# Kernel tuning notes

Measured on AMD Instinct MI355X. Metric: run time of the kernel, lower is better.

The kernel has to match this reference:

```python
import jax, jax.numpy as jnp
import numpy as np

LAMBDA_FGW = 0.5
TAU_KL = 0.1
N_OUTER = 5
N_SINKHORN = 10
DIM = 512


def _pdist(a, b):
    # sqrt(clamp(||a-b||^2, 1e-6)) computed via expansion (avoids BxKxMxD temp)
    n2 = ((a * a).sum(-1)[:, :, None] + (b * b).sum(-1)[:, None, :]
          - 2.0 * jnp.einsum('bkd,bmd->bkm', a, b))
    return jnp.sqrt(jnp.clip(n2, 1e-6, None))


def setup_inputs() -> dict:
    key = jax.random.key(0)
    ks = jax.random.split(key, 10)
    B, K, M, D = 256, 128, 128, DIM
    inp = {
        'sq': jax.random.normal(ks[0], (B, K, D), jnp.float32),
        'sr': jax.random.normal(ks[1], (B, M, D), jnp.float32),
        'mask_q': jax.random.uniform(ks[2], (B, K), jnp.float32),
        'mask_r': jax.random.uniform(ks[3], (B, M), jnp.float32),
        'centroids_q': jax.random.normal(ks[4], (B, K, D), jnp.float32),
        'centroids_r': jax.random.normal(ks[5], (B, M, D), jnp.float32),
        'W1': jax.random.normal(ks[6], (D, D), jnp.float32) * 0.02,
        'b1': jnp.zeros((D,), jnp.float32),
        'W2': jax.random.normal(ks[7], (D, D), jnp.float32) * 0.02,
        'b2': jnp.zeros((D,), jnp.float32),
        'log_eps': jnp.asarray(np.log(0.05), jnp.float32),
    }
    return inp


def reference(sq, sr, mask_q, mask_r, centroids_q, centroids_r, W1, b1, W2, b2, log_eps):
    proj = lambda x: jax.nn.relu(x @ W1 + b1) @ W2 + b2
    pq, pr = proj(sq), proj(sr)
    C = _pdist(pq, pr)                      # [B,K,M]
    Sq = _pdist(centroids_q, centroids_q)   # [B,K,K]
    Sr = _pdist(centroids_r, centroids_r)   # [B,M,M]

    mu = mask_q / (mask_q.sum(-1, keepdims=True) + 1e-8)  # [B,K]
    nu = mask_r / (mask_r.sum(-1, keepdims=True) + 1e-8)  # [B,M]
    T = mu[:, :, None] * nu[:, None, :]

    eps = jnp.clip(jnp.exp(log_eps), 0.01, 0.5)
    rho = TAU_KL / (TAU_KL + eps)
    log_mu = jnp.log(jnp.clip(mu, 1e-8, None))
    log_nu = jnp.log(jnp.clip(nu, 1e-8, None))
    Sq2, Sr2 = Sq * Sq, Sr * Sr

    C_fgw = C
    for _ in range(N_OUTER):
        t1 = jnp.einsum('bkl,bl->bk', Sq2, T.sum(2))[:, :, None]
        t2 = jnp.einsum('bm,bmn->bn', T.sum(1), Sr2)[:, None, :]
        L_gw = t1 + t2 - 2.0 * jnp.einsum('bkl,blm->bkm', Sq, jnp.einsum('blm,bmn->bln', T, Sr))
        C_fgw = (1.0 - LAMBDA_FGW) * C + LAMBDA_FGW * L_gw
        log_K = -C_fgw / eps
        log_u = jnp.zeros_like(mu)
        log_v = jnp.zeros_like(nu)
        for _ in range(N_SINKHORN):
            log_u = rho * (log_mu - jax.nn.logsumexp(log_K + log_v[:, None, :], axis=2))
            log_v = rho * (log_nu - jax.nn.logsumexp(log_K + log_u[:, :, None], axis=1))
        T = jnp.exp(log_u[:, :, None] + log_K + log_v[:, None, :])

    cost = (T * C_fgw).sum((-1, -2))
    similarity = jax.nn.sigmoid(-cost)
    return similarity, T, C, cost
```

## Files before the change

### kernel.cpp

```cpp
#include <hip/hip_runtime.h>
#include <math.h>

typedef unsigned short u16;
typedef __attribute__((ext_vector_type(4))) float f32x4;
typedef __attribute__((ext_vector_type(8))) short bf16x8;
typedef __attribute__((ext_vector_type(4))) unsigned short u16x4;
typedef __attribute__((ext_vector_type(8))) unsigned short u16x8;

#define DEVI static __device__ __forceinline__

DEVI float b2f(u16 u){ union{float f; unsigned i;} v; v.i = ((unsigned)u)<<16; return v.f; }
DEVI u16 f2b(float f){ union{float f; unsigned i;} v; v.f=f;
  unsigned r = v.i + 0x7fffu + ((v.i>>16)&1u); return (u16)(r>>16); }

DEVI void gload_lds16(const void* g, void* l){
  __builtin_amdgcn_global_load_lds((const __attribute__((address_space(1))) void*)g,
                                   (__attribute__((address_space(3))) void*)l, 16, 0, 0);
}

DEVI f32x4 vmax4(f32x4 a, f32x4 b){
  f32x4 r; r[0]=fmaxf(a[0],b[0]); r[1]=fmaxf(a[1],b[1]);
  r[2]=fmaxf(a[2],b[2]); r[3]=fmaxf(a[3],b[3]); return r;
}

__global__ void prepw_k(const float* __restrict__ W, u16* __restrict__ Wt){
  int id = blockIdx.x*256 + threadIdx.x;
  int k = id>>9, c = id&511;
  Wt[c*512 + k] = f2b(W[id]);
}

__global__ void cvt_k(const float* __restrict__ src, u16* __restrict__ dst,
                      float* __restrict__ norms, int nrows){
  int gw = (int)((blockIdx.x*blockDim.x + threadIdx.x)>>6);
  int lane = threadIdx.x & 63;
  if (gw >= nrows) return;
  const float* s = src + (size_t)gw*512;
  u16* d = dst + (size_t)gw*512;
  float acc = 0.f;
  #pragma unroll
  for (int q=0;q<2;q++){
    f32x4 v = *(const f32x4*)(s + q*256 + lane*4);
    u16x4 u;
    #pragma unroll
    for (int e=0;e<4;e++){
      u16 b = f2b(v[e]); u[e] = b;
      float fv = b2f(b); acc += fv*fv;
    }
    *(u16x4*)(d + q*256 + lane*4) = u;
  }
  #pragma unroll
  for (int off=1;off<64;off<<=1) acc += __shfl_xor(acc, off);
  if (norms != nullptr && lane==0) norms[gw] = acc;
}

__global__ void normb_k(const u16* __restrict__ src, float* __restrict__ norms, int nrows){
  int gw = (int)((blockIdx.x*blockDim.x + threadIdx.x)>>6);
  int lane = threadIdx.x & 63;
  if (gw >= nrows) return;
  const u16* s = src + (size_t)gw*512;
  u16x8 v = *(const u16x8*)(s + lane*8);
  float acc = 0.f;
  #pragma unroll
  for (int e=0;e<8;e++){ float f = b2f(v[e]); acc += f*f; }
  #pragma unroll
  for (int off=1;off<64;off<<=1) acc += __shfl_xor(acc, off);
  if (lane==0) norms[gw] = acc;
}

template<int ACT>
__global__ __launch_bounds__(256) void gemm_k(const u16* __restrict__ X,
    const u16* __restrict__ Wt, const float* __restrict__ bias, u16* __restrict__ OUT){
  __shared__ __align__(16) u16 sA[128*64];
  __shared__ __align__(16) u16 sB[128*64];
  const int tid = threadIdx.x, wave = tid>>6, lane = tid&63;
  const int bid = (blockIdx.x&7)*256 + (blockIdx.x>>3);
  const int rblk = bid>>2, cb = (bid&3)<<7;
  const u16* Xb = X + (size_t)rblk*(128*512);
  const u16* Wb = Wt + (size_t)cb*512;
  const int lrow = lane&15, lg = lane>>4, wr = wave>>1, wc = wave&1;
  f32x4 acc[4][4] = {};
  for (int s=0;s<8;s++){
    const int k0 = s<<6;
    #pragma unroll
    for (int q=0;q<4;q++){
      const int i = (wave<<2)+q;
      const int row = (i<<3) + (lane>>3);
      const int cd = (lane&7) ^ (row&7);
      gload_lds16(Xb + row*512 + k0 + (cd<<3), sA + i*512);
      gload_lds16(Wb + row*512 + k0 + (cd<<3), sB + i*512);
    }
    __syncthreads();
    #pragma unroll
    for (int kh=0;kh<2;kh++){
      bf16x8 a_[4], b_[4];
      #pragma unroll
      for (int i=0;i<4;i++){
        const int ra = (wr<<6)+(i<<4)+lrow;
        a_[i] = *(const bf16x8*)(sA + ra*64 + ((((kh<<2)+lg)^(ra&7))<<3));
        const int rb = (wc<<6)+(i<<4)+lrow;
        b_[i] = *(const bf16x8*)(sB + rb*64 + ((((kh<<2)+lg)^(rb&7))<<3));
      }
      #pragma unroll
      for (int i=0;i<4;i++)
        #pragma unroll
        for (int j=0;j<4;j++)
          acc[i][j] = __builtin_amdgcn_mfma_f32_16x16x32_bf16(a_[i], b_[j], acc[i][j], 0,0,0);
    }
    __syncthreads();
  }
  #pragma unroll
  for (int j=0;j<4;j++){
    const int col = cb + (wc<<6) + (j<<4) + lrow;
    const float bv = bias[col];
    #pragma unroll
    for (int i=0;i<4;i++){
      const int row0 = (rblk<<7) + (wr<<6) + (i<<4) + (lg<<2);
      #pragma unroll
      for (int r=0;r<4;r++){
        float v = acc[i][j][r] + bv;
        if (ACT) v = fmaxf(v, 0.f);
        OUT[(size_t)(row0+r)*512 + col] = f2b(v);
      }
    }
  }
}

template<int MODE>
__global__ __launch_bounds__(256) void pdist_k(const u16* __restrict__ Xa,
    const u16* __restrict__ Xb2, const float* __restrict__ na, const float* __restrict__ nb,
    float* __restrict__ OUT, float* __restrict__ S2t, char* __restrict__ SHL){
  __shared__ __align__(16) u16 sA[128*64];
  __shared__ __align__(16) u16 sB[128*64];
  const int tid = threadIdx.x, wave = tid>>6, lane = tid&63;
  const int b = blockIdx.x;
  const u16* Ab = Xa + (size_t)b*(128*512);
  const u16* Bb = Xb2 + (size_t)b*(128*512);
  const int lrow = lane&15, lg = lane>>4, wr = wave>>1, wc = wave&1;
  f32x4 acc[4][4] = {};
  for (int s=0;s<8;s++){
    const int k0 = s<<6;
    #pragma unroll
    for (int q=0;q<4;q++){
      const int i = (wave<<2)+q;
      const int row = (i<<3) + (lane>>3);
      const int cd = (lane&7) ^ (row&7);
      gload_lds16(Ab + row*512 + k0 + (cd<<3), sA + i*512);
      gload_lds16(Bb + row*512 + k0 + (cd<<3), sB + i*512);
    }
    __syncthreads();
    #pragma unroll
    for (int kh=0;kh<2;kh++){
      bf16x8 a_[4], b_[4];
      #pragma unroll
      for (int i=0;i<4;i++){
        const int ra = (wr<<6)+(i<<4)+lrow;
        a_[i] = *(const bf16x8*)(sA + ra*64 + ((((kh<<2)+lg)^(ra&7))<<3));
        const int rb = (wc<<6)+(i<<4)+lrow;
        b_[i] = *(const bf16x8*)(sB + rb*64 + ((((kh<<2)+lg)^(rb&7))<<3));
      }
      #pragma unroll
      for (int i=0;i<4;i++)
        #pragma unroll
        for (int j=0;j<4;j++)
          acc[i][j] = __builtin_amdgcn_mfma_f32_16x16x32_bf16(a_[i], b_[j], acc[i][j], 0,0,0);
    }
    __syncthreads();
  }
  #pragma unroll
  for (int j=0;j<4;j++){
    const int col = (wc<<6)+(j<<4)+lrow;
    const float nbv = nb[b*128+col];
    #pragma unroll
    for (int i=0;i<4;i++){
      const int row0 = (wr<<6)+(i<<4)+(lg<<2);
      float sv[4];
      #pragma unroll
      for (int r=0;r<4;r++){
        float n2 = na[b*128+row0+r] + nbv - 2.0f*acc[i][j][r];
        sv[r] = sqrtf(fmaxf(n2, 1e-6f));
      }
      if (MODE==0){
        #pragma unroll
        for (int r=0;r<4;r++)
          OUT[(size_t)b*16384 + (size_t)(row0+r)*128 + col] = sv[r];
      } else {
        u16x4 hi4, lo4; f32x4 s2q;
        #pragma unroll
        for (int r=0;r<4;r++){
          u16 h = f2b(sv[r]); hi4[r] = h;
          lo4[r] = f2b(sv[r] - b2f(h));
          s2q[r] = sv[r]*sv[r];
        }
        const int sa = col*256 + ((((row0>>3)^col)&15)<<4) + ((row0&7)<<1);
        char* base = SHL + (size_t)b*65536;
        *(u16x4*)(base + sa) = hi4;
        *(u16x4*)(base + 32768 + sa) = lo4;
        *(f32x4*)(S2t + (size_t)b*16384 + col*128 + row0) = s2q;
      }
    }
  }
}

__global__ void prep_k(const float* __restrict__ mask_q, const float* __restrict__ mask_r,
                       float* __restrict__ lmu, float* __restrict__ lnu,
                       float* __restrict__ mu, float* __restrict__ nu){
  int b = blockIdx.x, t = threadIdx.x;
  __shared__ float red[4];
  float mq = mask_q[b*128+t], mr = mask_r[b*128+t];
  float s1 = mq, s2 = mr;
  #pragma unroll
  for (int off=1;off<64;off<<=1){ s1 += __shfl_xor(s1,off); s2 += __shfl_xor(s2,off); }
  if ((t&63)==0){ red[t>>6] = s1; red[2+(t>>6)] = s2; }
  __syncthreads();
  float sumq = red[0]+red[1], sumr = red[2]+red[3];
  float muv = mq/(sumq+1e-8f), nuv = mr/(sumr+1e-8f);
  lmu[b*128+t] = __logf(fmaxf(muv,1e-8f));
  lnu[b*128+t] = __logf(fmaxf(nuv,1e-8f));
  mu[b*128+t] = muv;
  nu[b*128+t] = nuv;
}

__global__ __launch_bounds__(512,1) void fgw_loop_k(
    const char* __restrict__ SQHL, const char* __restrict__ SRHL,
    const float* __restrict__ SQ2, const float* __restrict__ SR2,
    const float* __restrict__ C_g,
    const float* __restrict__ MU, const float* __restrict__ NU,
    const float* __restrict__ LMU, const float* __restrict__ LNU,
    const float* __restrict__ log_eps,
    float* __restrict__ T_out, float* __restrict__ cost_out, float* __restrict__ sim_out)
{
  __shared__ __align__(16) char bufT[65536];
  __shared__ __align__(16) char bufS[65536];
  __shared__ __align__(16) float avs[128], bvs[128], t1s[128], t2s[128];
  __shared__ __align__(16) float lus[128], lvs[128];
  __shared__ float redc[8];

  const int b = blockIdx.x, tid = threadIdx.x;
  const int w = tid>>6, lane = tid&63, l15 = lane&15, lg = lane>>4;
  const char* SqHLb = SQHL + (size_t)b*65536;
  const char* SrHLb = SRHL + (size_t)b*65536;
  const float* Sq2b = SQ2 + (size_t)b*16384;
  const float* Sr2b = SR2 + (size_t)b*16384;
  const float* Cb   = C_g + (size_t)b*16384;
  const float* MUb  = MU + b*128;
  const float* NUb  = NU + b*128;

  float eps = __expf(log_eps[0]); eps = fminf(fmaxf(eps,0.01f),0.5f);
  const float rho = 0.1f/(0.1f+eps), inve = 1.0f/eps;

  const int kR = 16*w + l15;
  const int nC = kR;
  const int n0 = 16*w + 4*lg;
  const float lmuR = LMU[b*128+kR];
  const float lnuC = LNU[b*128+nC];
  const float muR  = MUb[kR];
  const float nuC  = NUb[nC];

  const int rowA256 = (16*w + l15)*256;
  const int glo2 = lg ^ (l15 & 3);
  const int ghi2 = l15 & 12;
  const int wtail = l15*256 + ((((2*w + (lg>>1)) ^ l15)&15)<<4) + ((lg&1)<<3);

  f32x4 lkR[8], lkC[8];
  float luR = 0.f, lvC = 0.f;

  for (int outer=0; outer<5; outer++){
    #pragma unroll
    for (int r2=0;r2<8;r2++)
      gload_lds16(SrHLb + r2*8192 + tid*16, bufS + r2*8192 + tid*16);
    {
      f32x4 avp = {0.f,0.f,0.f,0.f};
      float bvp = 0.f;
      #pragma unroll
      for (int q=0;q<8;q++){
        f32x4 TRq, TCq;
        if (outer==0){
          const f32x4 nu4 = *(const f32x4*)(NUb + 16*q + 4*lg);
          const f32x4 mu4 = *(const f32x4*)(MUb + 16*q + 4*lg);
          TRq = muR*nu4;
          TCq = mu4*nuC;
        } else {
          const f32x4 lv4 = *(const f32x4*)&lvs[16*q+4*lg];
          const f32x4 lu4 = *(const f32x4*)&lus[16*q+4*lg];
          #pragma unroll
          for (int e=0;e<4;e++){
            TRq[e] = __expf(lkR[q][e] + luR + lv4[e]);
            TCq[e] = __expf(lkC[q][e] + lu4[e] + lvC);
          }
        }
        u16x4 hi4, lo4;
        #pragma unroll
        for (int e=0;e<4;e++){
          u16 h = f2b(TRq[e]); hi4[e] = h;
          lo4[e] = f2b(TRq[e] - b2f(h));
        }
        const int sa = kR*256 + ((((2*q+(lg>>1)) ^ l15)&15)<<4) + ((lg&1)<<3);
        *(u16x4*)(bufT + sa) = hi4;
        *(u16x4*)(bufT + 32768 + sa) = lo4;
        avp += TRq;
        bvp += TCq[0]+TCq[1]+TCq[2]+TCq[3];
      }
      float av = avp[0]+avp[1]+avp[2]+avp[3];
      av += __shfl_xor(av,16); av += __shfl_xor(av,32);
      bvp += __shfl_xor(bvp,16); bvp += __shfl_xor(bvp,32);
      if (lg==0){ avs[kR] = av; bvs[nC] = bvp; }
    }
    __syncthreads();

    {
      const int k = tid>>2, q = tid&3;
      const float* r1 = Sq2b + k*128 + q*32;
      const float* r2p = Sr2b + k*128 + q*32;
      f32x4 a1 = {0.f,0.f,0.f,0.f}, a2 = {0.f,0.f,0.f,0.f};
      #pragma unroll
      for (int i=0;i<8;i++){
        a1 += (*(const f32x4*)(r1+4*i)) * (*(const f32x4*)(avs+q*32+4*i));
        a2 += (*(const f32x4*)(r2p+4*i)) * (*(const f32x4*)(bvs+q*32+4*i));
      }
      float s1 = a1[0]+a1[1]+a1[2]+a1[3];
      float s2 = a2[0]+a2[1]+a2[2]+a2[3];
      s1 += __shfl_xor(s1,1); s1 += __shfl_xor(s1,2);
      s2 += __shfl_xor(s2,1); s2 += __shfl_xor(s2,2);
      if (q==0){ t1s[k]=s1; t2s[k]=s2; }
    }
    f32x4 acc1[8] = {};
    #pragma unroll
    for (int qt=0;qt<4;qt++){
      const int colOff = (((4*qt) ^ ghi2) | glo2) << 4;
      const bf16x8 ahi = *(const bf16x8*)(bufT + rowA256 + colOff);
      const bf16x8 alo = *(const bf16x8*)(bufT + 32768 + rowA256 + colOff);
      const int bbase = l15*256 + colOff;
      #pragma unroll
      for (int nt=0;nt<8;nt++){
        const bf16x8 bhi = *(const bf16x8*)(bufS + nt*4096 + bbase);
        const bf16x8 blo = *(const bf16x8*)(bufS + 32768 + nt*4096 + bbase);
        acc1[nt] = __builtin_amdgcn_mfma_f32_16x16x32_bf16(ahi, bhi, acc1[nt], 0,0,0);
        acc1[nt] = __builtin_amdgcn_mfma_f32_16x16x32_bf16(ahi, blo, acc1[nt], 0,0,0);
        acc1[nt] = __builtin_amdgcn_mfma_f32_16x16x32_bf16(alo, bhi, acc1[nt], 0,0,0);
      }
    }
    __syncthreads();
    #pragma unroll
    for (int r2=0;r2<8;r2++)
      gload_lds16(SqHLb + r2*8192 + tid*16, bufS + r2*8192 + tid*16);
    #pragma unroll
    for (int nt=0;nt<8;nt++){
      u16x4 hi4, lo4;
      #pragma unroll
      for (int r=0;r<4;r++){
        u16 h = f2b(acc1[nt][r]); hi4[r] = h;
        lo4[r] = f2b(acc1[nt][r] - b2f(h));
      }
      const int sa = nt*4096 + wtail;
      *(u16x4*)(bufT + sa) = hi4;
      *(u16x4*)(bufT + 32768 + sa) = lo4;
    }
    __syncthreads();
    f32x4 acc2[8] = {};
    #pragma unroll
    for (int qt=0;qt<4;qt++){
      const int colOff = (((4*qt) ^ ghi2) | glo2) << 4;
      const bf16x8 ahi = *(const bf16x8*)(bufT + rowA256 + colOff);
      const bf16x8 alo = *(const bf16x8*)(bufT + 32768 + rowA256 + colOff);
      const int bbase = l15*256 + colOff;
      #pragma unroll
      for (int kt=0;kt<8;kt++){
        const bf16x8 bhi = *(const bf16x8*)(bufS + kt*4096 + bbase);
        const bf16x8 blo = *(const bf16x8*)(bufS + 32768 + kt*4096 + bbase);
        acc2[kt] = __builtin_amdgcn_mfma_f32_16x16x32_bf16(ahi, bhi, acc2[kt], 0,0,0);
        acc2[kt] = __builtin_amdgcn_mfma_f32_16x16x32_bf16(ahi, blo, acc2[kt], 0,0,0);
        acc2[kt] = __builtin_amdgcn_mfma_f32_16x16x32_bf16(alo, bhi, acc2[kt], 0,0,0);
      }
    }
    f32x4 lkf[8];
    {
      const f32x4 t24 = *(const f32x4*)&t2s[n0];
      #pragma unroll
      for (int kt=0;kt<8;kt++){
        const int k = 16*kt + l15;
        const f32x4 c4 = *(const f32x4*)(Cb + k*128 + n0);
        lkf[kt] = -inve*(0.5f*c4 + 0.5f*(t1s[k] + t24 - 2.0f*acc2[kt]));
      }
    }
    __syncthreads();
    #pragma unroll
    for (int kt=0;kt<8;kt++){
      const int row = 16*kt + l15;
      const int gp = ((4*w+lg) ^ (row&31)) & 31;
      *(f32x4*)(bufT + row*512 + gp*16) = lkf[kt];
      #pragma unroll
      for (int e=0;e<4;e++){
        const int n = n0 + e;
        const int gt = ((4*kt + (l15>>2)) ^ (n&31)) & 31;
        *(float*)(bufS + n*512 + gt*16 + (l15&3)*4) = lkf[kt][e];
      }
    }
    __syncthreads();
    #pragma unroll
    for (int q=0;q<8;q++){
      const int g1 = ((4*q+lg) ^ (kR&31)) & 31;
      lkR[q] = *(const f32x4*)(bufT + kR*512 + g1*16);
      const int g2 = ((4*q+lg) ^ (nC&31)) & 31;
      lkC[q] = *(const f32x4*)(bufS + nC*512 + g2*16);
    }
    for (int it=0; it<10; it++){
      f32x4 y[8];
      #pragma unroll
      for (int q=0;q<8;q++){
        if (it==0) y[q] = lkR[q];
        else       y[q] = lkR[q] + *(const f32x4*)&lvs[16*q+4*lg];
      }
      f32x4 m4 = y[0];
      #pragma unroll
      for (int q=1;q<8;q++) m4 = vmax4(m4, y[q]);
      float mx = fmaxf(fmaxf(m4[0],m4[1]), fmaxf(m4[2],m4[3]));
      mx = fmaxf(mx, __shfl_xor(mx,16));
      mx = fmaxf(mx, __shfl_xor(mx,32));
      f32x4 s4 = {0.f,0.f,0.f,0.f};
      #pragma unroll
      for (int q=0;q<8;q++){
        #pragma unroll
        for (int e=0;e<4;e++) s4[e] += __expf(y[q][e]-mx);
      }
      float s = s4[0]+s4[1]+s4[2]+s4[3];
      s += __shfl_xor(s,16); s += __shfl_xor(s,32);
      luR = rho*(lmuR - (mx + __logf(s)));
      if (lg==0) lus[kR] = luR;
      __syncthreads();
      #pragma unroll
      for (int q=0;q<8;q++)
        y[q] = lkC[q] + *(const f32x4*)&lus[16*q+4*lg];
      m4 = y[0];
      #pragma unroll
      for (int q=1;q<8;q++) m4 = vmax4(m4, y[q]);
      mx = fmaxf(fmaxf(m4[0],m4[1]), fmaxf(m4[2],m4[3]));
      mx = fmaxf(mx, __shfl_xor(mx,16));
      mx = fmaxf(mx, __shfl_xor(mx,32));
      s4 = (f32x4){0.f,0.f,0.f,0.f};
      #pragma unroll
      for (int q=0;q<8;q++){
        #pragma unroll
        for (int e=0;e<4;e++) s4[e] += __expf(y[q][e]-mx);
      }
      s = s4[0]+s4[1]+s4[2]+s4[3];
      s += __shfl_xor(s,16); s += __shfl_xor(s,32);
      lvC = rho*(lnuC - (mx + __logf(s)));
      if (lg==0) lvs[nC] = lvC;
      __syncthreads();
    }
    if (outer==4){
      float cp = 0.f;
      float* Tb = T_out + (size_t)b*16384;
      #pragma unroll
      for (int q=0;q<8;q++){
        const f32x4 lv4 = *(const f32x4*)&lvs[16*q+4*lg];
        f32x4 t;
        #pragma unroll
        for (int e=0;e<4;e++) t[e] = __expf(lkR[q][e] + luR + lv4[e]);
        *(f32x4*)(Tb + kR*128 + 16*q + 4*lg) = t;
        const f32x4 p = t*lkR[q];
        cp += p[0]+p[1]+p[2]+p[3];
      }
      cp *= -eps;
      #pragma unroll
      for (int off=1;off<64;off<<=1) cp += __shfl_xor(cp, off);
      if (lane==0) redc[w] = cp;
      __syncthreads();
      if (tid==0){
        float tot = 0.f;
        #pragma unroll
        for (int w2=0;w2<8;w2++) tot += redc[w2];
        cost_out[b] = tot;
        sim_out[b]  = 1.0f/(1.0f + __expf(tot));
      }
    }
  }
}

extern "C" void kernel_launch(void* const* d_in, const int* in_sizes, int n_in,
                              void* d_out, int out_size, void* d_ws, size_t ws_size,
                              hipStream_t stream){
  const float* sq      = (const float*)d_in[0];
  const float* sr      = (const float*)d_in[1];
  const float* mask_q  = (const float*)d_in[2];
  const float* mask_r  = (const float*)d_in[3];
  const float* cq      = (const float*)d_in[4];
  const float* cr      = (const float*)d_in[5];
  const float* W1      = (const float*)d_in[6];
  const float* b1      = (const float*)d_in[7];
  const float* W2      = (const float*)d_in[8];
  const float* b2      = (const float*)d_in[9];
  const float* log_eps = (const float*)d_in[10];

  float* out  = (float*)d_out;
  float* sim  = out;
  float* Tm   = out + 256;
  float* Cm   = Tm + 4194304;
  float* cost = Cm + 4194304;

  char* ws = (char*)d_ws;
  size_t off = 0;
  auto alloc = [&](size_t bytes)->void*{ void* p = ws + off; off += (bytes+255)&~(size_t)255; return p; };
  u16*   SQB = (u16*)  alloc(33554432);
  u16*   SRB = (u16*)  alloc(33554432);
  u16*   HQ  = (u16*)  alloc(33554432);
  u16*   HR  = (u16*)  alloc(33554432);
  u16*   W1T = (u16*)  alloc(524288);
  u16*   W2T = (u16*)  alloc(524288);
  float* NP  = (float*)alloc(262144);
  float* NCQ = (float*)alloc(131072);
  float* NCR = (float*)alloc(131072);
  float* LMU = (float*)alloc(131072);
  float* LNU = (float*)alloc(131072);
  float* MUA = (float*)alloc(131072);
  float* NUA = (float*)alloc(131072);
  (void)ws_size; (void)in_sizes; (void)n_in; (void)out_size;

  u16* PQ  = SQB;
  u16* CQB = HQ;
  u16* CRB = HR;

  float* SQ2  = (float*)((char*)SQB);
  float* SR2  = (float*)((char*)SQB + 16777216);
  char*  SQHL = (char*)SQB + 33554432;
  char*  SRHL = (char*)SQB + 50331648;

  prepw_k<<<1024,256,0,stream>>>(W1, W1T);
  prepw_k<<<1024,256,0,stream>>>(W2, W2T);
  cvt_k<<<8192,256,0,stream>>>(sq, SQB, nullptr, 32768);
  cvt_k<<<8192,256,0,stream>>>(sr, SRB, nullptr, 32768);
  gemm_k<1><<<2048,256,0,stream>>>(SQB, W1T, b1, HQ);
  gemm_k<0><<<2048,256,0,stream>>>(HQ, W2T, b2, PQ);
  normb_k<<<16384,256,0,stream>>>(PQ, NP, 65536);
  cvt_k<<<8192,256,0,stream>>>(cq, CQB, NCQ, 32768);
  cvt_k<<<8192,256,0,stream>>>(cr, CRB, NCR, 32768);
  pdist_k<0><<<256,256,0,stream>>>(PQ, PQ + (size_t)32768*512, NP, NP + 32768,
                                   Cm, nullptr, nullptr);
  pdist_k<1><<<256,256,0,stream>>>(CQB, CQB, NCQ, NCQ, nullptr, SQ2, SQHL);
  pdist_k<1><<<256,256,0,stream>>>(CRB, CRB, NCR, NCR, nullptr, SR2, SRHL);
  prep_k<<<256,128,0,stream>>>(mask_q, mask_r, LMU, LNU, MUA, NUA);
  fgw_loop_k<<<256,512,0,stream>>>(SQHL, SRHL, SQ2, SR2, Cm, MUA, NUA, LMU, LNU,
                                   log_eps, Tm, cost, sim);
}
```

Before: 477.4 us.

## Fuse MLP projection into one kernel and widen FGW loop to 1024 threads

```diff
diff --git a/kernel.cpp b/kernel.cpp
--- a/kernel.cpp
+++ b/kernel.cpp
@@ -26,7 +26,7 @@
 __global__ void prepw_k(const float* __restrict__ W, u16* __restrict__ Wt){
   int id = blockIdx.x*256 + threadIdx.x;
   int k = id>>9, c = id&511;
-  Wt[c*512 + k] = f2b(W[id]);
+  Wt[c*512 + (((k>>3)^(c&15))<<3) + (k&7)] = f2b(W[id]);
 }
 
 __global__ void cvt_k(const float* __restrict__ src, u16* __restrict__ dst,
@@ -50,78 +50,115 @@
   }
   #pragma unroll
   for (int off=1;off<64;off<<=1) acc += __shfl_xor(acc, off);
-  if (norms != nullptr && lane==0) norms[gw] = acc;
-}
-
-__global__ void normb_k(const u16* __restrict__ src, float* __restrict__ norms, int nrows){
-  int gw = (int)((blockIdx.x*blockDim.x + threadIdx.x)>>6);
-  int lane = threadIdx.x & 63;
-  if (gw >= nrows) return;
-  const u16* s = src + (size_t)gw*512;
-  u16x8 v = *(const u16x8*)(s + lane*8);
-  float acc = 0.f;
-  #pragma unroll
-  for (int e=0;e<8;e++){ float f = b2f(v[e]); acc += f*f; }
-  #pragma unroll
-  for (int off=1;off<64;off<<=1) acc += __shfl_xor(acc, off);
   if (lane==0) norms[gw] = acc;
 }
 
-template<int ACT>
-__global__ __launch_bounds__(256) void gemm_k(const u16* __restrict__ X,
-    const u16* __restrict__ Wt, const float* __restrict__ bias, u16* __restrict__ OUT){
-  __shared__ __align__(16) u16 sA[128*64];
-  __shared__ __align__(16) u16 sB[128*64];
-  const int tid = threadIdx.x, wave = tid>>6, lane = tid&63;
-  const int bid = (blockIdx.x&7)*256 + (blockIdx.x>>3);
-  const int rblk = bid>>2, cb = (bid&3)<<7;
-  const u16* Xb = X + (size_t)rblk*(128*512);
-  const u16* Wb = Wt + (size_t)cb*512;
-  const int lrow = lane&15, lg = lane>>4, wr = wave>>1, wc = wave&1;
-  f32x4 acc[4][4] = {};
-  for (int s=0;s<8;s++){
-    const int k0 = s<<6;
-    #pragma unroll
-    for (int q=0;q<4;q++){
-      const int i = (wave<<2)+q;
-      const int row = (i<<3) + (lane>>3);
-      const int cd = (lane&7) ^ (row&7);
-      gload_lds16(Xb + row*512 + k0 + (cd<<3), sA + i*512);
-      gload_lds16(Wb + row*512 + k0 + (cd<<3), sB + i*512);
-    }
-    __syncthreads();
-    #pragma unroll
-    for (int kh=0;kh<2;kh++){
-      bf16x8 a_[4], b_[4];
-      #pragma unroll
-      for (int i=0;i<4;i++){
-        const int ra = (wr<<6)+(i<<4)+lrow;
-        a_[i] = *(const bf16x8*)(sA + ra*64 + ((((kh<<2)+lg)^(ra&7))<<3));
-        const int rb = (wc<<6)+(i<<4)+lrow;
-        b_[i] = *(const bf16x8*)(sB + rb*64 + ((((kh<<2)+lg)^(rb&7))<<3));
-      }
+__global__ __launch_bounds__(512) void mlp_k(
+    const float* __restrict__ sq, const float* __restrict__ sr,
+    const u16* __restrict__ W1S, const u16* __restrict__ W2S,
+    const float* __restrict__ b1, const float* __restrict__ b2,
+    u16* __restrict__ P, float* __restrict__ NP)
+{
+  __shared__ __align__(16) u16 sW[2][16384];
+  __shared__ __align__(16) u16 sH[64*512];
+  __shared__ float sB1[512], sB2[512];
+  __shared__ float npart[8][16];
+
+  const int tid = threadIdx.x, w = tid>>6, lane = tid&63;
+  const int l15 = lane&15, lg = lane>>4;
+  const int rt = w>>1, par = w&1;
+  const int row0 = blockIdx.x*64;
+  const float* Xb = (blockIdx.x < 512) ? sq + (size_t)row0*512
+                                       : sr + (size_t)(row0-32768)*512;
+  if (tid<512){ sB1[tid] = b1[tid]; sB2[tid] = b2[tid]; }
+
+  bf16x8 Xfr[16];
+  {
+    const float* xr = Xb + (size_t)(16*rt + l15)*512;
+    #pragma unroll
+    for (int kc=0;kc<16;kc++){
+      f32x4 a = *(const f32x4*)(xr + 32*kc + 8*lg);
+      f32x4 c2 = *(const f32x4*)(xr + 32*kc + 8*lg + 4);
+      u16x8 t;
+      t[0]=f2b(a[0]); t[1]=f2b(a[1]); t[2]=f2b(a[2]); t[3]=f2b(a[3]);
+      t[4]=f2b(c2[0]); t[5]=f2b(c2[1]); t[6]=f2b(c2[2]); t[7]=f2b(c2[3]);
+      Xfr[kc] = *(bf16x8*)&t;
+    }
+  }
+
+  #pragma unroll
+  for (int i=0;i<4;i++)
+    gload_lds16((const char*)W1S + i*8192 + tid*16, (char*)sW[0] + i*8192 + tid*16);
+  __syncthreads();
+  for (int p=0;p<16;p++){
+    if (p<15){
       #pragma unroll
       for (int i=0;i<4;i++)
-        #pragma unroll
-        for (int j=0;j<4;j++)
-          acc[i][j] = __builtin_amdgcn_mfma_f32_16x16x32_bf16(a_[i], b_[j], acc[i][j], 0,0,0);
-    }
-    __syncthreads();
-  }
-  #pragma unroll
-  for (int j=0;j<4;j++){
-    const int col = cb + (wc<<6) + (j<<4) + lrow;
-    const float bv = bias[col];
-    #pragma unroll
-    for (int i=0;i<4;i++){
-      const int row0 = (rblk<<7) + (wr<<6) + (i<<4) + (lg<<2);
-      #pragma unroll
-      for (int r=0;r<4;r++){
-        float v = acc[i][j][r] + bv;
-        if (ACT) v = fmaxf(v, 0.f);
-        OUT[(size_t)(row0+r)*512 + col] = f2b(v);
-      }
-    }
+        gload_lds16((const char*)W1S + (p+1)*32768 + i*8192 + tid*16,
+                    (char*)sW[(p+1)&1] + i*8192 + tid*16);
+    }
+    f32x4 acc = {0.f,0.f,0.f,0.f};
+    const u16* bw = sW[p&1] + (16*par + l15)*512;
+    #pragma unroll
+    for (int kc=0;kc<16;kc++){
+      bf16x8 bf = *(const bf16x8*)(bw + (((4*kc+lg)^l15)<<3));
+      acc = __builtin_amdgcn_mfma_f32_16x16x32_bf16(Xfr[kc], bf, acc, 0,0,0);
+    }
+    const int c = 32*p + 16*par + l15;
+    const float bv = sB1[c];
+    #pragma unroll
+    for (int r=0;r<4;r++){
+      float h = fmaxf(acc[r]+bv, 0.f);
+      const int m = 16*rt + 4*lg + r;
+      sH[m*512 + (((c>>3)^(m&15))<<3) + (c&7)] = f2b(h);
+    }
+    __syncthreads();
+  }
+
+  f32x4 nacc = {0.f,0.f,0.f,0.f};
+  #pragma unroll
+  for (int i=0;i<4;i++)
+    gload_lds16((const char*)W2S + i*8192 + tid*16, (char*)sW[0] + i*8192 + tid*16);
+  __syncthreads();
+  for (int p=0;p<16;p++){
+    if (p<15){
+      #pragma unroll
+      for (int i=0;i<4;i++)
+        gload_lds16((const char*)W2S + (p+1)*32768 + i*8192 + tid*16,
+                    (char*)sW[(p+1)&1] + i*8192 + tid*16);
+    }
+    f32x4 acc = {0.f,0.f,0.f,0.f};
+    const u16* bw = sW[p&1] + (16*par + l15)*512;
+    const u16* ar = sH + (16*rt + l15)*512;
+    #pragma unroll
+    for (int kc=0;kc<16;kc++){
+      bf16x8 af = *(const bf16x8*)(ar + (((4*kc+lg)^l15)<<3));
+      bf16x8 bf = *(const bf16x8*)(bw + (((4*kc+lg)^l15)<<3));
+      acc = __builtin_amdgcn_mfma_f32_16x16x32_bf16(af, bf, acc, 0,0,0);
+    }
+    const int c = 32*p + 16*par + l15;
+    const float bv = sB2[c];
+    #pragma unroll
+    for (int r=0;r<4;r++){
+      float pv = acc[r]+bv;
+      u16 pb = f2b(pv);
+      const int m = 16*rt + 4*lg + r;
+      P[(size_t)(row0+m)*512 + c] = pb;
+      float fv = b2f(pb);
+      nacc[r] += fv*fv;
+    }
+    __syncthreads();
+  }
+  #pragma unroll
+  for (int off=1;off<16;off<<=1){
+    nacc[0] += __shfl_xor(nacc[0],off); nacc[1] += __shfl_xor(nacc[1],off);
+    nacc[2] += __shfl_xor(nacc[2],off); nacc[3] += __shfl_xor(nacc[3],off);
+  }
+  if (l15==0) *(f32x4*)&npart[w][4*lg] = nacc;
+  __syncthreads();
+  if (tid<64){
+    int rt2 = tid>>4, m = tid&15;
+    NP[row0 + 16*rt2 + m] = npart[2*rt2][m] + npart[2*rt2+1][m];
   }
 }
 
@@ -202,7 +239,7 @@
 }
 
 __global__ void prep_k(const float* __restrict__ mask_q, const float* __restrict__ mask_r,
-                       float* __restrict__ lmu, float* __restrict__ lnu,
+                       float* __restrict__ lmu2, float* __restrict__ lnu2,
                        float* __restrict__ mu, float* __restrict__ nu){
   int b = blockIdx.x, t = threadIdx.x;
   __shared__ float red[4];
@@ -214,18 +251,18 @@
   __syncthreads();
   float sumq = red[0]+red[1], sumr = red[2]+red[3];
   float muv = mq/(sumq+1e-8f), nuv = mr/(sumr+1e-8f);
-  lmu[b*128+t] = __logf(fmaxf(muv,1e-8f));
-  lnu[b*128+t] = __logf(fmaxf(nuv,1e-8f));
+  lmu2[b*128+t] = __log2f(fmaxf(muv,1e-8f));
+  lnu2[b*128+t] = __log2f(fmaxf(nuv,1e-8f));
   mu[b*128+t] = muv;
   nu[b*128+t] = nuv;
 }
 
-__global__ __launch_bounds__(512,1) void fgw_loop_k(
+__global__ __launch_bounds__(1024,1) void fgw_loop_k(
     const char* __restrict__ SQHL, const char* __restrict__ SRHL,
     const float* __restrict__ SQ2, const float* __restrict__ SR2,
     const float* __restrict__ C_g,
     const float* __restrict__ MU, const float* __restrict__ NU,
-    const float* __restrict__ LMU, const float* __restrict__ LNU,
+    const float* __restrict__ LMU2, const float* __restrict__ LNU2,
     const float* __restrict__ log_eps,
     float* __restrict__ T_out, float* __restrict__ cost_out, float* __restrict__ sim_out)
 {
@@ -233,10 +270,12 @@
   __shared__ __align__(16) char bufS[65536];
   __shared__ __align__(16) float avs[128], bvs[128], t1s[128], t2s[128];
   __shared__ __align__(16) float lus[128], lvs[128];
-  __shared__ float redc[8];
+  __shared__ float redc[16];
 
   const int b = blockIdx.x, tid = threadIdx.x;
   const int w = tid>>6, lane = tid&63, l15 = lane&15, lg = lane>>4;
+  const int l7 = lane&7, p8 = lane>>3;
+  const int at = w>>1, par = w&1;
   const char* SqHLb = SQHL + (size_t)b*65536;
   const char* SrHLb = SRHL + (size_t)b*65536;
   const float* Sq2b = SQ2 + (size_t)b*16384;
@@ -246,222 +285,217 @@
   const float* NUb  = NU + b*128;
 
   float eps = __expf(log_eps[0]); eps = fminf(fmaxf(eps,0.01f),0.5f);
-  const float rho = 0.1f/(0.1f+eps), inve = 1.0f/eps;
-
-  const int kR = 16*w + l15;
-  const int nC = kR;
-  const int n0 = 16*w + 4*lg;
-  const float lmuR = LMU[b*128+kR];
-  const float lnuC = LNU[b*128+nC];
-  const float muR  = MUb[kR];
-  const float nuC  = NUb[nC];
-
-  const int rowA256 = (16*w + l15)*256;
-  const int glo2 = lg ^ (l15 & 3);
-  const int ghi2 = l15 & 12;
-  const int wtail = l15*256 + ((((2*w + (lg>>1)) ^ l15)&15)<<4) + ((lg&1)<<3);
-
-  f32x4 lkR[8], lkC[8];
+  const float rho = 0.1f/(0.1f+eps);
+  const float inve2 = 1.4426950408889634f/eps;
+
+  const int kR = 8*w + l7;
+  const float lmu2R = LMU2[b*128+kR];
+  const float lnu2C = LNU2[b*128+kR];
+  const int n0 = 16*at + 4*lg;
+
+  f32x4 lkR[4], lkC[4];
   float luR = 0.f, lvC = 0.f;
 
   for (int outer=0; outer<5; outer++){
     #pragma unroll
-    for (int r2=0;r2<8;r2++)
-      gload_lds16(SrHLb + r2*8192 + tid*16, bufS + r2*8192 + tid*16);
+    for (int i=0;i<4;i++)
+      gload_lds16(SrHLb + i*16384 + tid*16, bufS + i*16384 + tid*16);
+
     {
       f32x4 avp = {0.f,0.f,0.f,0.f};
       float bvp = 0.f;
       #pragma unroll
-      for (int q=0;q<8;q++){
-        f32x4 TRq, TCq;
+      for (int jj=0;jj<4;jj++){
+        f32x4 TR, TC;
         if (outer==0){
-          const f32x4 nu4 = *(const f32x4*)(NUb + 16*q + 4*lg);
-          const f32x4 mu4 = *(const f32x4*)(MUb + 16*q + 4*lg);
-          TRq = muR*nu4;
-          TCq = mu4*nuC;
+          const f32x4 nu4 = *(const f32x4*)(NUb + 16*p8 + 4*jj);
+          const f32x4 mu4 = *(const f32x4*)(MUb + 16*p8 + 4*jj);
+          const float muR = MUb[kR], nuC = NUb[kR];
+          TR = muR*nu4; TC = mu4*nuC;
         } else {
-          const f32x4 lv4 = *(const f32x4*)&lvs[16*q+4*lg];
-          const f32x4 lu4 = *(const f32x4*)&lus[16*q+4*lg];
+          const f32x4 lv4 = *(const f32x4*)&lvs[16*p8 + 4*jj];
+          const f32x4 lu4 = *(const f32x4*)&lus[16*p8 + 4*jj];
           #pragma unroll
           for (int e=0;e<4;e++){
-            TRq[e] = __expf(lkR[q][e] + luR + lv4[e]);
-            TCq[e] = __expf(lkC[q][e] + lu4[e] + lvC);
+            TR[e] = exp2f(lkR[jj][e] + luR + lv4[e]);
+            TC[e] = exp2f(lkC[jj][e] + lu4[e] + lvC);
           }
         }
         u16x4 hi4, lo4;
         #pragma unroll
         for (int e=0;e<4;e++){
-          u16 h = f2b(TRq[e]); hi4[e] = h;
-          lo4[e] = f2b(TRq[e] - b2f(h));
+          u16 h = f2b(TR[e]); hi4[e] = h;
+          lo4[e] = f2b(TR[e] - b2f(h));
         }
-        const int sa = kR*256 + ((((2*q+(lg>>1)) ^ l15)&15)<<4) + ((lg&1)<<3);
+        const int sa = kR*256 + ((((2*p8+(jj>>1))^(kR&15)))<<4) + ((jj&1)<<3);
         *(u16x4*)(bufT + sa) = hi4;
         *(u16x4*)(bufT + 32768 + sa) = lo4;
-        avp += TRq;
-        bvp += TCq[0]+TCq[1]+TCq[2]+TCq[3];
+        avp += TR;
+        bvp += TC[0]+TC[1]+TC[2]+TC[3];
       }
       float av = avp[0]+avp[1]+avp[2]+avp[3];
-      av += __shfl_xor(av,16); av += __shfl_xor(av,32);
-      bvp += __shfl_xor(bvp,16); bvp += __shfl_xor(bvp,32);
-      if (lg==0){ avs[kR] = av; bvs[nC] = bvp; }
-    }
-    __syncthreads();
-
+      av += __shfl_xor(av,8); av += __shfl_xor(av,16); av += __shfl_xor(av,32);
+      bvp += __shfl_xor(bvp,8); bvp += __shfl_xor(bvp,16); bvp += __shfl_xor(bvp,32);
+      if (p8==0){ avs[kR] = av; bvs[kR] = bvp; }
+    }
+    __syncthreads();
+
+    f32x4 Cf[4];
+    #pragma unroll
+    for (int j=0;j<4;j++)
+      Cf[j] = *(const f32x4*)(Cb + (size_t)(16*(4*par+j)+l15)*128 + n0);
     {
-      const int k = tid>>2, q = tid&3;
-      const float* r1 = Sq2b + k*128 + q*32;
-      const float* r2p = Sr2b + k*128 + q*32;
+      const int k = tid>>3, sub = tid&7;
+      const float* r1 = Sq2b + k*128 + 16*sub;
+      const float* r2p = Sr2b + k*128 + 16*sub;
       f32x4 a1 = {0.f,0.f,0.f,0.f}, a2 = {0.f,0.f,0.f,0.f};
       #pragma unroll
-      for (int i=0;i<8;i++){
-        a1 += (*(const f32x4*)(r1+4*i)) * (*(const f32x4*)(avs+q*32+4*i));
-        a2 += (*(const f32x4*)(r2p+4*i)) * (*(const f32x4*)(bvs+q*32+4*i));
+      for (int i=0;i<4;i++){
+        a1 += (*(const f32x4*)(r1+4*i)) * (*(const f32x4*)(avs+16*sub+4*i));
+        a2 += (*(const f32x4*)(r2p+4*i)) * (*(const f32x4*)(bvs+16*sub+4*i));
       }
       float s1 = a1[0]+a1[1]+a1[2]+a1[3];
       float s2 = a2[0]+a2[1]+a2[2]+a2[3];
-      s1 += __shfl_xor(s1,1); s1 += __shfl_xor(s1,2);
-      s2 += __shfl_xor(s2,1); s2 += __shfl_xor(s2,2);
-      if (q==0){ t1s[k]=s1; t2s[k]=s2; }
-    }
-    f32x4 acc1[8] = {};
+      s1 += __shfl_xor(s1,1); s1 += __shfl_xor(s1,2); s1 += __shfl_xor(s1,4);
+      s2 += __shfl_xor(s2,1); s2 += __shfl_xor(s2,2); s2 += __shfl_xor(s2,4);
+      if (sub==0){ t1s[k]=s1; t2s[k]=s2; }
+    }
+    f32x4 acc1[4] = {};
     #pragma unroll
     for (int qt=0;qt<4;qt++){
-      const int colOff = (((4*qt) ^ ghi2) | glo2) << 4;
-      const bf16x8 ahi = *(const bf16x8*)(bufT + rowA256 + colOff);
-      const bf16x8 alo = *(const bf16x8*)(bufT + 32768 + rowA256 + colOff);
-      const int bbase = l15*256 + colOff;
-      #pragma unroll
-      for (int nt=0;nt<8;nt++){
-        const bf16x8 bhi = *(const bf16x8*)(bufS + nt*4096 + bbase);
-        const bf16x8 blo = *(const bf16x8*)(bufS + 32768 + nt*4096 + bbase);
-        acc1[nt] = __builtin_amdgcn_mfma_f32_16x16x32_bf16(ahi, bhi, acc1[nt], 0,0,0);
-        acc1[nt] = __builtin_amdgcn_mfma_f32_16x16x32_bf16(ahi, blo, acc1[nt], 0,0,0);
-        acc1[nt] = __builtin_amdgcn_mfma_f32_16x16x32_bf16(alo, bhi, acc1[nt], 0,0,0);
-      }
-    }
-    __syncthreads();
-    #pragma unroll
-    for (int r2=0;r2<8;r2++)
-      gload_lds16(SqHLb + r2*8192 + tid*16, bufS + r2*8192 + tid*16);
-    #pragma unroll
-    for (int nt=0;nt<8;nt++){
+      const int aoff = (16*at+l15)*256 + (((4*qt+lg)^l15)<<4);
+      const bf16x8 ahi = *(const bf16x8*)(bufT + aoff);
+      const bf16x8 alo = *(const bf16x8*)(bufT + 32768 + aoff);
+      #pragma unroll
+      for (int j=0;j<4;j++){
+        const int boff = (16*(4*par+j)+l15)*256 + (((4*qt+lg)^l15)<<4);
+        const bf16x8 bhi = *(const bf16x8*)(bufS + boff);
+        const bf16x8 blo = *(const bf16x8*)(bufS + 32768 + boff);
+        acc1[j] = __builtin_amdgcn_mfma_f32_16x16x32_bf16(ahi, bhi, acc1[j], 0,0,0);
+        acc1[j] = __builtin_amdgcn_mfma_f32_16x16x32_bf16(ahi, blo, acc1[j], 0,0,0);
+        acc1[j] = __builtin_amdgcn_mfma_f32_16x16x32_bf16(alo, bhi, acc1[j], 0,0,0);
+      }
+    }
+    __syncthreads();
+
+    #pragma unroll
+    for (int i=0;i<4;i++)
+      gload_lds16(SqHLb + i*16384 + tid*16, bufS + i*16384 + tid*16);
+    #pragma unroll
+    for (int j=0;j<4;j++){
       u16x4 hi4, lo4;
       #pragma unroll
       for (int r=0;r<4;r++){
-        u16 h = f2b(acc1[nt][r]); hi4[r] = h;
-        lo4[r] = f2b(acc1[nt][r] - b2f(h));
-      }
-      const int sa = nt*4096 + wtail;
+        u16 h = f2b(acc1[j][r]); hi4[r] = h;
+        lo4[r] = f2b(acc1[j][r] - b2f(h));
+      }
+      const int sa = (16*(4*par+j)+l15)*256 + ((((2*at+(lg>>1))^l15))<<4) + ((lg&1)<<3);
       *(u16x4*)(bufT + sa) = hi4;
       *(u16x4*)(bufT + 32768 + sa) = lo4;
     }
     __syncthreads();
-    f32x4 acc2[8] = {};
+
+    f32x4 acc2[4] = {};
     #pragma unroll
     for (int qt=0;qt<4;qt++){
-      const int colOff = (((4*qt) ^ ghi2) | glo2) << 4;
-      const bf16x8 ahi = *(const bf16x8*)(bufT + rowA256 + colOff);
-      const bf16x8 alo = *(const bf16x8*)(bufT + 32768 + rowA256 + colOff);
-      const int bbase = l15*256 + colOff;
-      #pragma unroll
-      for (int kt=0;kt<8;kt++){
-        const bf16x8 bhi = *(const bf16x8*)(bufS + kt*4096 + bbase);
-        const bf16x8 blo = *(const bf16x8*)(bufS + 32768 + kt*4096 + bbase);
-        acc2[kt] = __builtin_amdgcn_mfma_f32_16x16x32_bf16(ahi, bhi, acc2[kt], 0,0,0);
-        acc2[kt] = __builtin_amdgcn_mfma_f32_16x16x32_bf16(ahi, blo, acc2[kt], 0,0,0);
-        acc2[kt] = __builtin_amdgcn_mfma_f32_16x16x32_bf16(alo, bhi, acc2[kt], 0,0,0);
-      }
-    }
-    f32x4 lkf[8];
+      const int aoff = (16*at+l15)*256 + (((4*qt+lg)^l15)<<4);
+      const bf16x8 ahi = *(const bf16x8*)(bufT + aoff);
+      const bf16x8 alo = *(const bf16x8*)(bufT + 32768 + aoff);
+      #pragma unroll
+      for (int j=0;j<4;j++){
+        const int boff = (16*(4*par+j)+l15)*256 + (((4*qt+lg)^l15)<<4);
+        const bf16x8 bhi = *(const bf16x8*)(bufS + boff);
+        const bf16x8 blo = *(const bf16x8*)(bufS + 32768 + boff);
+        acc2[j] = __builtin_amdgcn_mfma_f32_16x16x32_bf16(ahi, bhi, acc2[j], 0,0,0);
+        acc2[j] = __builtin_amdgcn_mfma_f32_16x16x32_bf16(ahi, blo, acc2[j], 0,0,0);
+        acc2[j] = __builtin_amdgcn_mfma_f32_16x16x32_bf16(alo, bhi, acc2[j], 0,0,0);
+      }
+    }
+    f32x4 lkf[4];
     {
       const f32x4 t24 = *(const f32x4*)&t2s[n0];
       #pragma unroll
-      for (int kt=0;kt<8;kt++){
-        const int k = 16*kt + l15;
-        const f32x4 c4 = *(const f32x4*)(Cb + k*128 + n0);
-        lkf[kt] = -inve*(0.5f*c4 + 0.5f*(t1s[k] + t24 - 2.0f*acc2[kt]));
-      }
-    }
-    __syncthreads();
-    #pragma unroll
-    for (int kt=0;kt<8;kt++){
-      const int row = 16*kt + l15;
-      const int gp = ((4*w+lg) ^ (row&31)) & 31;
-      *(f32x4*)(bufT + row*512 + gp*16) = lkf[kt];
-      #pragma unroll
-      for (int e=0;e<4;e++){
-        const int n = n0 + e;
-        const int gt = ((4*kt + (l15>>2)) ^ (n&31)) & 31;
-        *(float*)(bufS + n*512 + gt*16 + (l15&3)*4) = lkf[kt][e];
-      }
-    }
-    __syncthreads();
-    #pragma unroll
-    for (int q=0;q<8;q++){
-      const int g1 = ((4*q+lg) ^ (kR&31)) & 31;
-      lkR[q] = *(const f32x4*)(bufT + kR*512 + g1*16);
-      const int g2 = ((4*q+lg) ^ (nC&31)) & 31;
-      lkC[q] = *(const f32x4*)(bufS + nC*512 + g2*16);
-    }
+      for (int j=0;j<4;j++){
+        const float t1v = t1s[16*(4*par+j)+l15];
+        lkf[j] = -inve2*(0.5f*Cf[j] + 0.5f*(t1v + t24 - 2.0f*acc2[j]));
+      }
+    }
+    __syncthreads();
+
+    #pragma unroll
+    for (int j=0;j<4;j++){
+      const int kj = 16*(4*par+j)+l15;
+      *(f32x4*)(bufT + kj*512 + (((4*at+lg)^(kj&31))<<4)) = lkf[j];
+      #pragma unroll
+      for (int r=0;r<4;r++){
+        const int n = n0 + r;
+        *(float*)(bufS + n*512 + ((((16*par+4*j+(l15>>2))^(n&31)))<<4) + ((l15&3)<<2))
+          = lkf[j][r];
+      }
+    }
+    __syncthreads();
+    #pragma unroll
+    for (int jj=0;jj<4;jj++){
+      lkR[jj] = *(const f32x4*)(bufT + kR*512 + (((4*p8+jj)^(kR&31))<<4));
+      lkC[jj] = *(const f32x4*)(bufS + kR*512 + (((4*p8+jj)^(kR&31))<<4));
+    }
+
     for (int it=0; it<10; it++){
-      f32x4 y[8];
-      #pragma unroll
-      for (int q=0;q<8;q++){
-        if (it==0) y[q] = lkR[q];
-        else       y[q] = lkR[q] + *(const f32x4*)&lvs[16*q+4*lg];
-      }
-      f32x4 m4 = y[0];
-      #pragma unroll
-      for (int q=1;q<8;q++) m4 = vmax4(m4, y[q]);
+      f32x4 y[4];
+      #pragma unroll
+      for (int jj=0;jj<4;jj++){
+        y[jj] = lkR[jj];
+        if (it) y[jj] += *(const f32x4*)&lvs[16*p8+4*jj];
+      }
+      f32x4 m4 = vmax4(vmax4(y[0],y[1]), vmax4(y[2],y[3]));
       float mx = fmaxf(fmaxf(m4[0],m4[1]), fmaxf(m4[2],m4[3]));
-      mx = fmaxf(mx, __shfl_xor(mx,16));
-      mx = fmaxf(mx, __shfl_xor(mx,32));
+      mx = fmaxf(mx,__shfl_xor(mx,8)); mx = fmaxf(mx,__shfl_xor(mx,16));
+      mx = fmaxf(mx,__shfl_xor(mx,32));
       f32x4 s4 = {0.f,0.f,0.f,0.f};
       #pragma unroll
-      for (int q=0;q<8;q++){
-        #pragma unroll
-        for (int e=0;e<4;e++) s4[e] += __expf(y[q][e]-mx);
+      for (int jj=0;jj<4;jj++){
+        #pragma unroll
+        for (int e=0;e<4;e++) s4[e] += exp2f(y[jj][e]-mx);
       }
       float s = s4[0]+s4[1]+s4[2]+s4[3];
-      s += __shfl_xor(s,16); s += __shfl_xor(s,32);
-      luR = rho*(lmuR - (mx + __logf(s)));
-      if (lg==0) lus[kR] = luR;
+      s += __shfl_xor(s,8); s += __shfl_xor(s,16); s += __shfl_xor(s,32);
+      luR = rho*(lmu2R - (mx + __log2f(s)));
+      if (p8==0) lus[kR] = luR;
       __syncthreads();
       #pragma unroll
-      for (int q=0;q<8;q++)
-        y[q] = lkC[q] + *(const f32x4*)&lus[16*q+4*lg];
-      m4 = y[0];
-      #pragma unroll
-      for (int q=1;q<8;q++) m4 = vmax4(m4, y[q]);
+      for (int jj=0;jj<4;jj++)
+        y[jj] = lkC[jj] + *(const f32x4*)&lus[16*p8+4*jj];
+      m4 = vmax4(vmax4(y[0],y[1]), vmax4(y[2],y[3]));
       mx = fmaxf(fmaxf(m4[0],m4[1]), fmaxf(m4[2],m4[3]));
-      mx = fmaxf(mx, __shfl_xor(mx,16));
-      mx = fmaxf(mx, __shfl_xor(mx,32));
+      mx = fmaxf(mx,__shfl_xor(mx,8)); mx = fmaxf(mx,__shfl_xor(mx,16));
+      mx = fmaxf(mx,__shfl_xor(mx,32));
       s4 = (f32x4){0.f,0.f,0.f,0.f};
       #pragma unroll
-      for (int q=0;q<8;q++){
-        #pragma unroll
-        for (int e=0;e<4;e++) s4[e] += __expf(y[q][e]-mx);
+      for (int jj=0;jj<4;jj++){
+        #pragma unroll
+        for (int e=0;e<4;e++) s4[e] += exp2f(y[jj][e]-mx);
       }
       s = s4[0]+s4[1]+s4[2]+s4[3];
-      s += __shfl_xor(s,16); s += __shfl_xor(s,32);
-      lvC = rho*(lnuC - (mx + __logf(s)));
-      if (lg==0) lvs[nC] = lvC;
+      s += __shfl_xor(s,8); s += __shfl_xor(s,16); s += __shfl_xor(s,32);
+      lvC = rho*(lnu2C - (mx + __log2f(s)));
+      if (p8==0) lvs[kR] = lvC;
       __syncthreads();
     }
+
     if (outer==4){
       float cp = 0.f;
       float* Tb = T_out + (size_t)b*16384;
       #pragma unroll
-      for (int q=0;q<8;q++){
-        const f32x4 lv4 = *(const f32x4*)&lvs[16*q+4*lg];
+      for (int jj=0;jj<4;jj++){
+        const f32x4 lv4 = *(const f32x4*)&lvs[16*p8+4*jj];
         f32x4 t;
         #pragma unroll
-        for (int e=0;e<4;e++) t[e] = __expf(lkR[q][e] + luR + lv4[e]);
-        *(f32x4*)(Tb + kR*128 + 16*q + 4*lg) = t;
-        const f32x4 p = t*lkR[q];
-        cp += p[0]+p[1]+p[2]+p[3];
-      }
-      cp *= -eps;
+        for (int e=0;e<4;e++) t[e] = exp2f(lkR[jj][e] + luR + lv4[e]);
+        *(f32x4*)(Tb + kR*128 + 16*p8 + 4*jj) = t;
+        const f32x4 pr = t*lkR[jj];
+        cp += pr[0]+pr[1]+pr[2]+pr[3];
+      }
+      cp *= -eps*0.6931471805599453f;
       #pragma unroll
       for (int off=1;off<64;off<<=1) cp += __shfl_xor(cp, off);
       if (lane==0) redc[w] = cp;
@@ -469,7 +503,7 @@
       if (tid==0){
         float tot = 0.f;
         #pragma unroll
-        for (int w2=0;w2<8;w2++) tot += redc[w2];
+        for (int w2=0;w2<16;w2++) tot += redc[w2];
         cost_out[b] = tot;
         sim_out[b]  = 1.0f/(1.0f + __expf(tot));
       }
@@ -501,12 +535,11 @@
   char* ws = (char*)d_ws;
   size_t off = 0;
   auto alloc = [&](size_t bytes)->void*{ void* p = ws + off; off += (bytes+255)&~(size_t)255; return p; };
-  u16*   SQB = (u16*)  alloc(33554432);
-  u16*   SRB = (u16*)  alloc(33554432);
-  u16*   HQ  = (u16*)  alloc(33554432);
-  u16*   HR  = (u16*)  alloc(33554432);
-  u16*   W1T = (u16*)  alloc(524288);
-  u16*   W2T = (u16*)  alloc(524288);
+  u16*   P   = (u16*)  alloc(67108864);
+  u16*   CQB = (u16*)  alloc(33554432);
+  u16*   CRB = (u16*)  alloc(33554432);
+  u16*   W1S = (u16*)  alloc(524288);
+  u16*   W2S = (u16*)  alloc(524288);
   float* NP  = (float*)alloc(262144);
   float* NCQ = (float*)alloc(131072);
   float* NCR = (float*)alloc(131072);
@@ -516,29 +549,21 @@
   float* NUA = (float*)alloc(131072);
   (void)ws_size; (void)in_sizes; (void)n_in; (void)out_size;
 
-  u16* PQ  = SQB;
-  u16* CQB = HQ;
-  u16* CRB = HR;
-
-  float* SQ2  = (float*)((char*)SQB);
-  float* SR2  = (float*)((char*)SQB + 16777216);
-  char*  SQHL = (char*)SQB + 33554432;
-  char*  SRHL = (char*)SQB + 50331648;
-
-  prepw_k<<<1024,256,0,stream>>>(W1, W1T);
-  prepw_k<<<1024,256,0,stream>>>(W2, W2T);
-  cvt_k<<<8192,256,0,stream>>>(sq, SQB, nullptr, 32768);
-  cvt_k<<<8192,256,0,stream>>>(sr, SRB, nullptr, 32768);
-  gemm_k<1><<<2048,256,0,stream>>>(SQB, W1T, b1, HQ);
-  gemm_k<0><<<2048,256,0,stream>>>(HQ, W2T, b2, PQ);
-  normb_k<<<16384,256,0,stream>>>(PQ, NP, 65536);
+  float* SQ2  = (float*)((char*)P);
+  float* SR2  = (float*)((char*)P + 16777216);
+  char*  SQHL = (char*)P + 33554432;
+  char*  SRHL = (char*)P + 50331648;
+
+  prepw_k<<<1024,256,0,stream>>>(W1, W1S);
+  prepw_k<<<1024,256,0,stream>>>(W2, W2S);
   cvt_k<<<8192,256,0,stream>>>(cq, CQB, NCQ, 32768);
   cvt_k<<<8192,256,0,stream>>>(cr, CRB, NCR, 32768);
-  pdist_k<0><<<256,256,0,stream>>>(PQ, PQ + (size_t)32768*512, NP, NP + 32768,
+  mlp_k<<<1024,512,0,stream>>>(sq, sr, W1S, W2S, b1, b2, P, NP);
+  pdist_k<0><<<256,256,0,stream>>>(P, P + (size_t)32768*512, NP, NP + 32768,
                                    Cm, nullptr, nullptr);
   pdist_k<1><<<256,256,0,stream>>>(CQB, CQB, NCQ, NCQ, nullptr, SQ2, SQHL);
   pdist_k<1><<<256,256,0,stream>>>(CRB, CRB, NCR, NCR, nullptr, SR2, SRHL);
   prep_k<<<256,128,0,stream>>>(mask_q, mask_r, LMU, LNU, MUA, NUA);
-  fgw_loop_k<<<256,512,0,stream>>>(SQHL, SRHL, SQ2, SR2, Cm, MUA, NUA, LMU, LNU,
-                                   log_eps, Tm, cost, sim);
-}
+  fgw_loop_k<<<256,1024,0,stream>>>(SQHL, SRHL, SQ2, SR2, Cm, MUA, NUA, LMU, LNU,
+                                    log_eps, Tm, cost, sim);
+}
```

Result: slower. 541.1 us (+13.3%).
